# Optimization experiments

Measured on AMD Instinct MI355X. Metric: run time of the kernel, lower is better.

The kernel has to match this reference:

```python
import jax, jax.numpy as jnp
import numpy as np

H, W = 128, 128
TANFOVX = 0.5
TANFOVY = 0.5
SCALE_MOD = 1.0
NEAR = 0.2
N = 2048


def setup_inputs() -> dict:
    key = jax.random.key(0)
    ks = jax.random.split(key, 6)
    # Gaussians in front of an identity camera looking down +z
    xy = jax.random.uniform(ks[0], (N, 2), minval=-1.5, maxval=1.5)
    z = jax.random.uniform(ks[1], (N, 1), minval=2.5, maxval=6.5)
    means3D = jnp.concatenate([xy, z], axis=1).astype(jnp.float32)
    opacities = jax.random.uniform(ks[2], (N, 1), minval=0.05, maxval=0.95)
    colors_precomp = jax.random.uniform(ks[3], (N, 3))
    scales = jax.random.uniform(ks[4], (N, 3), minval=0.01, maxval=0.06)
    rotations = jax.random.normal(ks[5], (N, 4))
    viewmatrix = jnp.eye(4, dtype=jnp.float32)  # world == camera frame
    bg = jnp.zeros((3,), dtype=jnp.float32)
    return dict(means3D=means3D, opacities=opacities,
                colors_precomp=colors_precomp, scales=scales,
                rotations=rotations, viewmatrix=viewmatrix, bg=bg)


def _quat_to_rot(q):
    # normalized quaternion (w, x, y, z) -> rotation matrix, as in the CUDA kernel
    q = q / jnp.linalg.norm(q, axis=-1, keepdims=True)
    w, x, y, z = q[:, 0], q[:, 1], q[:, 2], q[:, 3]
    return jnp.stack([
        jnp.stack([1 - 2 * (y * y + z * z), 2 * (x * y - w * z), 2 * (x * z + w * y)], -1),
        jnp.stack([2 * (x * y + w * z), 1 - 2 * (x * x + z * z), 2 * (y * z - w * x)], -1),
        jnp.stack([2 * (x * z - w * y), 2 * (y * z + w * x), 1 - 2 * (x * x + y * y)], -1),
    ], -2)  # [N,3,3]


def _forward(means3D, opacities, colors_precomp, scales, rotations, viewmatrix, bg):
    fx = W / (2.0 * TANFOVX)
    fy = H / (2.0 * TANFOVY)
    Rv = viewmatrix[:3, :3]
    tv = viewmatrix[:3, 3]
    pv = means3D @ Rv.T + tv            # view-space positions [N,3]
    x, y, z = pv[:, 0], pv[:, 1], pv[:, 2]
    zc = jnp.maximum(z, 1e-4)
    # frustum clamping of the EWA Jacobian, as in forward.cu
    tx = jnp.clip(x / zc, -1.3 * TANFOVX, 1.3 * TANFOVX) * zc
    ty = jnp.clip(y / zc, -1.3 * TANFOVY, 1.3 * TANFOVY) * zc
    zeros = jnp.zeros_like(zc)
    J = jnp.stack([
        jnp.stack([fx / zc, zeros, -fx * tx / (zc * zc)], -1),
        jnp.stack([zeros, fy / zc, -fy * ty / (zc * zc)], -1),
    ], -2)                               # [N,2,3]
    # 3D covariance Sigma = R S S^T R^T
    Rg = _quat_to_rot(rotations)
    M = Rg * (scales * SCALE_MOD)[:, None, :]
    Sigma = M @ jnp.swapaxes(M, -1, -2)  # [N,3,3]
    T2 = jnp.einsum('nij,jk->nik', J, Rv)
    cov2d = jnp.einsum('nij,njk,nlk->nil', T2, Sigma, T2)
    a = cov2d[:, 0, 0] + 0.3             # low-pass filter, as in CUDA
    b = cov2d[:, 0, 1]
    c = cov2d[:, 1, 1] + 0.3
    det = a * c - b * b
    valid = (det > 0) & (z > NEAR)
    inv_det = jnp.where(det != 0, 1.0 / det, 0.0)
    conA, conB, conC = c * inv_det, -b * inv_det, a * inv_det
    mid = 0.5 * (a + c)
    lam = mid + jnp.sqrt(jnp.maximum(mid * mid - det, 0.1))
    radii = jnp.where(valid, jnp.ceil(3.0 * jnp.sqrt(lam)), 0.0)
    # projected pixel-space means
    mx = fx * (x / zc) + 0.5 * (W - 1)
    my = fy * (y / zc) + 0.5 * (H - 1)

    # global front-to-back depth sort (CUDA sorts per tile; one tile here)
    order = jnp.argsort(z)
    mx_s, my_s = mx[order], my[order]
    A_s, B_s, C_s = conA[order], conB[order], conC[order]
    op_s = opacities[order, 0]
    z_s = z[order]
    col_s = colors_precomp[order]
    valid_s = valid[order]

    px = jnp.arange(W, dtype=means3D.dtype)
    py = jnp.arange(H, dtype=means3D.dtype)
    Dx = mx_s[None, :] - px[:, None]     # [W,N]
    Dy = my_s[None, :] - py[:, None]     # [H,N]
    # power = -0.5 (A dx^2 + C dy^2) - B dx dy, built [H,W,N]
    power = (-0.5 * A_s * Dx * Dx)[None, :, :] \
            + (-0.5 * C_s * Dy * Dy)[:, None, :] \
            - (B_s * Dx)[None, :, :] * Dy[:, None, :]
    alpha = jnp.minimum(0.99, op_s * jnp.exp(jnp.minimum(power, 0.0)))
    alpha = jnp.where((power <= 0.0) & valid_s & (alpha >= 1.0 / 255.0), alpha, 0.0)
    alpha = alpha.reshape(H * W, N)      # [HW,N], front-to-back order
    logt = jnp.log1p(-alpha)
    csum = jnp.cumsum(logt, axis=-1)
    T_excl = jnp.exp(csum - logt)        # exclusive transmittance prod_{j<i}(1-a_j)
    wgt = alpha * T_excl                 # compositing weights
    T_final = jnp.exp(csum[:, -1])
    color = jnp.einsum('pn,nc->cp', wgt, col_s).reshape(3, H, W) \
            + T_final.reshape(1, H, W) * bg[:, None, None]
    depth = (wgt * z_s[None, :]).sum(-1).reshape(H, W)
    alpha_img = (1.0 - T_final).reshape(H, W)
    return color, radii, depth, alpha_img


def reference(means3D, opacities, colors_precomp, scales, rotations, viewmatrix, bg):
    return _forward(means3D, opacities, colors_precomp, scales, rotations, viewmatrix, bg)
```

## Files before the change

### kernel.cpp

```cpp
#include <hip/hip_runtime.h>

#define NG    2048
#define IMG_W 128
#define IMG_H 128
#define NPIX  (IMG_W * IMG_H)
#define REC   12

__global__ __launch_bounds__(64) void preprocess_kernel(
    const float* __restrict__ means,
    const float* __restrict__ opac,
    const float* __restrict__ cols,
    const float* __restrict__ scales,
    const float* __restrict__ rots,
    const float* __restrict__ vm4,
    float* __restrict__ u,
    float* __restrict__ zkey,
    float* __restrict__ radii_out)
{
    int i = blockIdx.x * 64 + threadIdx.x;
    if (i >= NG) return;

    const double fx = 128.0, fy = 128.0;

    double R00 = vm4[0], R01 = vm4[1], R02 = vm4[2],  t0 = vm4[3];
    double R10 = vm4[4], R11 = vm4[5], R12 = vm4[6],  t1 = vm4[7];
    double R20 = vm4[8], R21 = vm4[9], R22 = vm4[10], t2 = vm4[11];

    double m0 = means[3*i+0], m1 = means[3*i+1], m2 = means[3*i+2];
    double x = R00*m0 + R01*m1 + R02*m2 + t0;
    double y = R10*m0 + R11*m1 + R12*m2 + t1;
    double z = R20*m0 + R21*m1 + R22*m2 + t2;

    double zc   = fmax(z, 1e-4);
    double invz = 1.0 / zc;
    const double limx = 1.3 * 0.5, limy = 1.3 * 0.5;
    double tx = fmin(limx, fmax(-limx, x * invz)) * zc;
    double ty = fmin(limy, fmax(-limy, y * invz)) * zc;

    double J00 = fx * invz, J02 = -fx * tx * invz * invz;
    double J11 = fy * invz, J12 = -fy * ty * invz * invz;

    double qw = rots[4*i+0], qx = rots[4*i+1], qy = rots[4*i+2], qz = rots[4*i+3];
    double qn = 1.0 / sqrt(qw*qw + qx*qx + qy*qy + qz*qz);
    qw *= qn; qx *= qn; qy *= qn; qz *= qn;

    double Rg00 = 1.0 - 2.0*(qy*qy + qz*qz), Rg01 = 2.0*(qx*qy - qw*qz), Rg02 = 2.0*(qx*qz + qw*qy);
    double Rg10 = 2.0*(qx*qy + qw*qz), Rg11 = 1.0 - 2.0*(qx*qx + qz*qz), Rg12 = 2.0*(qy*qz - qw*qx);
    double Rg20 = 2.0*(qx*qz - qw*qy), Rg21 = 2.0*(qy*qz + qw*qx), Rg22 = 1.0 - 2.0*(qx*qx + qy*qy);

    double s0 = scales[3*i+0], s1 = scales[3*i+1], s2 = scales[3*i+2];
    double M00 = Rg00*s0, M01 = Rg01*s1, M02 = Rg02*s2;
    double M10 = Rg10*s0, M11 = Rg11*s1, M12 = Rg12*s2;
    double M20 = Rg20*s0, M21 = Rg21*s1, M22 = Rg22*s2;

    double S00 = M00*M00 + M01*M01 + M02*M02;
    double S01 = M00*M10 + M01*M11 + M02*M12;
    double S02 = M00*M20 + M01*M21 + M02*M22;
    double S11 = M10*M10 + M11*M11 + M12*M12;
    double S12 = M10*M20 + M11*M21 + M12*M22;
    double S22 = M20*M20 + M21*M21 + M22*M22;

    double Ta0 = J00*R00 + J02*R20, Ta1 = J00*R01 + J02*R21, Ta2 = J00*R02 + J02*R22;
    double Tb0 = J11*R10 + J12*R20, Tb1 = J11*R11 + J12*R21, Tb2 = J11*R12 + J12*R22;

    double Ua0 = Ta0*S00 + Ta1*S01 + Ta2*S02;
    double Ua1 = Ta0*S01 + Ta1*S11 + Ta2*S12;
    double Ua2 = Ta0*S02 + Ta1*S12 + Ta2*S22;
    double Ub0 = Tb0*S00 + Tb1*S01 + Tb2*S02;
    double Ub1 = Tb0*S01 + Tb1*S11 + Tb2*S12;
    double Ub2 = Tb0*S02 + Tb1*S12 + Tb2*S22;
    double cov00 = Ua0*Ta0 + Ua1*Ta1 + Ua2*Ta2;
    double cov01 = Ua0*Tb0 + Ua1*Tb1 + Ua2*Tb2;
    double cov11 = Ub0*Tb0 + Ub1*Tb1 + Ub2*Tb2;

    double a = cov00 + 0.3;
    double b = cov01;
    double c = cov11 + 0.3;
    double det = a*c - b*b;
    bool valid = (det > 0.0) && (z > 0.2);
    double inv_det = (det != 0.0) ? (1.0 / det) : 0.0;
    double conA =  c * inv_det;
    double conB = -b * inv_det;
    double conC =  a * inv_det;
    double mid = 0.5 * (a + c);
    double lam = mid + sqrt(fmax(mid*mid - det, 0.1));
    float radii = valid ? (float)ceil(3.0 * sqrt(lam)) : 0.0f;

    double mx = fx * (x * invz) + 0.5 * (IMG_W - 1);
    double my = fy * (y * invz) + 0.5 * (IMG_H - 1);

    double op = valid ? (double)opac[i] : 0.0;

    double r2c = -1.0;
    if (op > 0.0) {
        double lnterm = log(255.0 * op);
        if (lnterm > 0.0) r2c = 2.0 * lnterm * lam * 1.0001 + 1e-3;
    }

    u[i*REC + 0]  = (float)mx;
    u[i*REC + 1]  = (float)my;
    u[i*REC + 2]  = (float)conA;
    u[i*REC + 3]  = (float)conB;
    u[i*REC + 4]  = (float)conC;
    u[i*REC + 5]  = (float)op;
    u[i*REC + 6]  = (float)z;
    u[i*REC + 7]  = cols[3*i+0];
    u[i*REC + 8]  = cols[3*i+1];
    u[i*REC + 9]  = cols[3*i+2];
    u[i*REC + 10] = (float)r2c;
    u[i*REC + 11] = 0.0f;
    zkey[i]       = (float)z;
    radii_out[i]  = radii;
}

__global__ __launch_bounds__(256) void rank_scatter_kernel(
    const float* __restrict__ u,
    const float* __restrict__ zkey,
    float* __restrict__ s,
    float4* __restrict__ key4)
{
    __shared__ float zl[NG];
    int tid = threadIdx.x;
    for (int j = tid; j < NG; j += 256) zl[j] = zkey[j];
    __syncthreads();

    int g = tid >> 4;
    int p = tid & 15;
    int i = blockIdx.x * 16 + g;
    float zi = zl[i];

    const float4* z4 = (const float4*)zl;
    int rank = 0;
    #pragma unroll 4
    for (int it = 0; it < 32; ++it) {
        int idx = it * 16 + p;
        float4 f = z4[idx];
        int j0 = idx * 4;
        rank += (f.x < zi) || (f.x == zi && (j0 + 0) < i);
        rank += (f.y < zi) || (f.y == zi && (j0 + 1) < i);
        rank += (f.z < zi) || (f.z == zi && (j0 + 2) < i);
        rank += (f.w < zi) || (f.w == zi && (j0 + 3) < i);
    }
    rank += __shfl_down(rank, 8, 16);
    rank += __shfl_down(rank, 4, 16);
    rank += __shfl_down(rank, 2, 16);
    rank += __shfl_down(rank, 1, 16);

    if (p == 0) {
        const float4* src = (const float4*)(u + (size_t)i * REC);
        float4 a0 = src[0], a1 = src[1], a2 = src[2];
        float4* dst = (float4*)(s + (size_t)rank * REC);
        dst[0] = a0; dst[1] = a1; dst[2] = a2;
        key4[rank] = make_float4(a0.x, a0.y, a2.z, 0.0f);
    }
}

__global__ __launch_bounds__(256) void composite_kernel(
    const float* __restrict__ s,
    const float4* __restrict__ key4,
    const float* __restrict__ bg,
    float* __restrict__ out)
{
    __shared__ float comb[4 * 64 * 5];

    int tid  = threadIdx.x;
    int lane = tid & 63;
    int w    = tid >> 6;
    int tile = blockIdx.x;
    int x0 = (tile & 15) * 8;
    int y0 = (tile >> 4) * 8;
    float x0f = (float)x0,       y0f = (float)y0;
    float x1f = (float)(x0 + 7), y1f = (float)(y0 + 7);

    int px = x0 + (lane & 7);
    int py = y0 + (lane >> 3);
    float fpx = (float)px, fpy = (float)py;
    int p = py * IMG_W + px;

    float cr = 0.f, cg = 0.f, cb = 0.f, dep = 0.f, T = 1.f;

    const int SEG = NG / 4;
    int segbase = w * SEG;
    for (int c = 0; c < SEG; c += 64) {
        int gi = segbase + c + lane;
        float4 k4 = key4[gi];
        float ddx = fmaxf(0.f, fmaxf(x0f - k4.x, k4.x - x1f));
        float ddy = fmaxf(0.f, fmaxf(y0f - k4.y, k4.y - y1f));
        bool pass = (ddx*ddx + ddy*ddy) <= k4.z;

        unsigned long long m = __ballot(pass);
        float4 a0 = make_float4(0.f,0.f,0.f,0.f);
        float4 a1 = a0;
        float2 a2 = make_float2(0.f,0.f);
        if (pass) {
            const float* r = s + (size_t)gi * REC;
            a0 = *(const float4*)(r);
            a1 = *(const float4*)(r + 4);
            a2 = *(const float2*)(r + 8);
        }
        while (m) {
            int b = __ffsll(m) - 1;
            m &= m - 1;
            float mx = __shfl(a0.x, b);
            float my = __shfl(a0.y, b);
            float A  = __shfl(a0.z, b);
            float B  = __shfl(a0.w, b);
            float C  = __shfl(a1.x, b);
            float op = __shfl(a1.y, b);
            float gz = __shfl(a1.z, b);
            float gr = __shfl(a1.w, b);
            float gg = __shfl(a2.x, b);
            float gb = __shfl(a2.y, b);
            float dx = mx - fpx;
            float dy = my - fpy;
            float power = -0.5f * (A*dx*dx + C*dy*dy) - B*dx*dy;
            if (power <= 0.0f) {
                float al = fminf(0.99f, op * __expf(power));
                if (al >= (1.0f / 255.0f)) {
                    float wg = al * T;
                    dep += wg * gz;
                    cr  += wg * gr;
                    cg  += wg * gg;
                    cb  += wg * gb;
                    T *= (1.0f - al);
                }
            }
        }
    }

    int cb_base = (w * 64 + lane) * 5;
    comb[cb_base + 0] = cr;
    comb[cb_base + 1] = cg;
    comb[cb_base + 2] = cb;
    comb[cb_base + 3] = dep;
    comb[cb_base + 4] = T;
    __syncthreads();

    if (w == 0) {
        float CR = 0.f, CG = 0.f, CB = 0.f, DEP = 0.f, TT = 1.f;
        #pragma unroll
        for (int ww = 0; ww < 4; ++ww) {
            int b2 = (ww * 64 + lane) * 5;
            CR  += TT * comb[b2 + 0];
            CG  += TT * comb[b2 + 1];
            CB  += TT * comb[b2 + 2];
            DEP += TT * comb[b2 + 3];
            TT  *= comb[b2 + 4];
        }
        out[0*NPIX + p] = CR + TT * bg[0];
        out[1*NPIX + p] = CG + TT * bg[1];
        out[2*NPIX + p] = CB + TT * bg[2];
        out[3*NPIX + NG + p]        = DEP;
        out[3*NPIX + NG + NPIX + p] = 1.f - TT;
    }
}

extern "C" void kernel_launch(void* const* d_in, const int* in_sizes, int n_in,
                              void* d_out, int out_size, void* d_ws, size_t ws_size,
                              hipStream_t stream)
{
    const float* means = (const float*)d_in[0];
    const float* opac  = (const float*)d_in[1];
    const float* cols  = (const float*)d_in[2];
    const float* scl   = (const float*)d_in[3];
    const float* rot   = (const float*)d_in[4];
    const float* vm    = (const float*)d_in[5];
    const float* bg    = (const float*)d_in[6];
    float* out = (float*)d_out;

    float*  u    = (float*)d_ws;
    float*  zkey = u + NG * REC;
    float*  s    = zkey + NG;
    float4* key4 = (float4*)(s + NG * REC);

    preprocess_kernel<<<NG / 64, 64, 0, stream>>>(
        means, opac, cols, scl, rot, vm, u, zkey, out + 3 * NPIX);
    rank_scatter_kernel<<<NG / 16, 256, 0, stream>>>(u, zkey, s, key4);
    composite_kernel<<<NPIX / 64, 256, 0, stream>>>(s, key4, bg, out);
}
```

Measured before the change: 26.09 us.

## Fuse preprocess into rank kernel and batch culling ballots in composite

Merges the preprocess and rank/scatter kernels into one launch. Each block recomputes view-space depth for all Gaussians into shared memory, ranks them, then one lane per Gaussian runs the full preprocess and writes the sorted record directly, which removes the intermediate buffer and one kernel launch. The composite kernel now computes all eight tile-culling ballots up front, and it loads the color and depth shuffles only when some lane in the wave actually contributes. The cost is redundant depth recomputation in every block and a serial preprocess done by only one lane out of sixteen.

```diff
diff --git a/kernel.cpp b/kernel.cpp
--- a/kernel.cpp
+++ b/kernel.cpp
@@ -6,25 +6,55 @@
 #define NPIX  (IMG_W * IMG_H)
 #define REC   12
 
-__global__ __launch_bounds__(64) void preprocess_kernel(
+__global__ __launch_bounds__(256) void prep_rank_kernel(
     const float* __restrict__ means,
     const float* __restrict__ opac,
     const float* __restrict__ cols,
     const float* __restrict__ scales,
     const float* __restrict__ rots,
     const float* __restrict__ vm4,
-    float* __restrict__ u,
-    float* __restrict__ zkey,
+    float* __restrict__ s,
+    float4* __restrict__ key4,
     float* __restrict__ radii_out)
 {
-    int i = blockIdx.x * 64 + threadIdx.x;
-    if (i >= NG) return;
+    __shared__ __align__(16) float zl[NG];
+    int tid = threadIdx.x;
 
     const double fx = 128.0, fy = 128.0;
 
     double R00 = vm4[0], R01 = vm4[1], R02 = vm4[2],  t0 = vm4[3];
     double R10 = vm4[4], R11 = vm4[5], R12 = vm4[6],  t1 = vm4[7];
     double R20 = vm4[8], R21 = vm4[9], R22 = vm4[10], t2 = vm4[11];
+
+    for (int j = tid; j < NG; j += 256) {
+        double zj = R20*means[3*j] + R21*means[3*j+1] + R22*means[3*j+2] + t2;
+        zl[j] = (float)zj;
+    }
+    __syncthreads();
+
+    int g = tid >> 4;
+    int p = tid & 15;
+    int i = blockIdx.x * 16 + g;
+    float zi = zl[i];
+
+    const float4* z4 = (const float4*)zl;
+    int rank = 0;
+    #pragma unroll 4
+    for (int it = 0; it < 32; ++it) {
+        int idx = it * 16 + p;
+        float4 f = z4[idx];
+        int j0 = idx * 4;
+        rank += (f.x < zi) || (f.x == zi && (j0 + 0) < i);
+        rank += (f.y < zi) || (f.y == zi && (j0 + 1) < i);
+        rank += (f.z < zi) || (f.z == zi && (j0 + 2) < i);
+        rank += (f.w < zi) || (f.w == zi && (j0 + 3) < i);
+    }
+    rank += __shfl_down(rank, 8, 16);
+    rank += __shfl_down(rank, 4, 16);
+    rank += __shfl_down(rank, 2, 16);
+    rank += __shfl_down(rank, 1, 16);
+
+    if (p != 0) return;
 
     double m0 = means[3*i+0], m1 = means[3*i+1], m2 = means[3*i+2];
     double x = R00*m0 + R01*m1 + R02*m2 + t0;
@@ -97,62 +127,12 @@
         if (lnterm > 0.0) r2c = 2.0 * lnterm * lam * 1.0001 + 1e-3;
     }
 
-    u[i*REC + 0]  = (float)mx;
-    u[i*REC + 1]  = (float)my;
-    u[i*REC + 2]  = (float)conA;
-    u[i*REC + 3]  = (float)conB;
-    u[i*REC + 4]  = (float)conC;
-    u[i*REC + 5]  = (float)op;
-    u[i*REC + 6]  = (float)z;
-    u[i*REC + 7]  = cols[3*i+0];
-    u[i*REC + 8]  = cols[3*i+1];
-    u[i*REC + 9]  = cols[3*i+2];
-    u[i*REC + 10] = (float)r2c;
-    u[i*REC + 11] = 0.0f;
-    zkey[i]       = (float)z;
-    radii_out[i]  = radii;
-}
-
-__global__ __launch_bounds__(256) void rank_scatter_kernel(
-    const float* __restrict__ u,
-    const float* __restrict__ zkey,
-    float* __restrict__ s,
-    float4* __restrict__ key4)
-{
-    __shared__ float zl[NG];
-    int tid = threadIdx.x;
-    for (int j = tid; j < NG; j += 256) zl[j] = zkey[j];
-    __syncthreads();
-
-    int g = tid >> 4;
-    int p = tid & 15;
-    int i = blockIdx.x * 16 + g;
-    float zi = zl[i];
-
-    const float4* z4 = (const float4*)zl;
-    int rank = 0;
-    #pragma unroll 4
-    for (int it = 0; it < 32; ++it) {
-        int idx = it * 16 + p;
-        float4 f = z4[idx];
-        int j0 = idx * 4;
-        rank += (f.x < zi) || (f.x == zi && (j0 + 0) < i);
-        rank += (f.y < zi) || (f.y == zi && (j0 + 1) < i);
-        rank += (f.z < zi) || (f.z == zi && (j0 + 2) < i);
-        rank += (f.w < zi) || (f.w == zi && (j0 + 3) < i);
-    }
-    rank += __shfl_down(rank, 8, 16);
-    rank += __shfl_down(rank, 4, 16);
-    rank += __shfl_down(rank, 2, 16);
-    rank += __shfl_down(rank, 1, 16);
-
-    if (p == 0) {
-        const float4* src = (const float4*)(u + (size_t)i * REC);
-        float4 a0 = src[0], a1 = src[1], a2 = src[2];
-        float4* dst = (float4*)(s + (size_t)rank * REC);
-        dst[0] = a0; dst[1] = a1; dst[2] = a2;
-        key4[rank] = make_float4(a0.x, a0.y, a2.z, 0.0f);
-    }
+    float* dst = s + (size_t)rank * REC;
+    *(float4*)(dst)     = make_float4((float)mx, (float)my, (float)conA, (float)conB);
+    *(float4*)(dst + 4) = make_float4((float)conC, (float)op, (float)z, cols[3*i+0]);
+    *(float4*)(dst + 8) = make_float4(cols[3*i+1], cols[3*i+2], (float)r2c, 0.0f);
+    key4[rank]   = make_float4((float)mx, (float)my, (float)r2c, 0.0f);
+    radii_out[i] = radii;
 }
 
 __global__ __launch_bounds__(256) void composite_kernel(
@@ -177,53 +157,61 @@
     float fpx = (float)px, fpy = (float)py;
     int p = py * IMG_W + px;
 
-    float cr = 0.f, cg = 0.f, cb = 0.f, dep = 0.f, T = 1.f;
-
     const int SEG = NG / 4;
     int segbase = w * SEG;
-    for (int c = 0; c < SEG; c += 64) {
-        int gi = segbase + c + lane;
-        float4 k4 = key4[gi];
+
+    unsigned long long m[8];
+    unsigned pb = 0;
+    #pragma unroll
+    for (int c = 0; c < 8; ++c) {
+        float4 k4 = key4[segbase + c * 64 + lane];
         float ddx = fmaxf(0.f, fmaxf(x0f - k4.x, k4.x - x1f));
         float ddy = fmaxf(0.f, fmaxf(y0f - k4.y, k4.y - y1f));
         bool pass = (ddx*ddx + ddy*ddy) <= k4.z;
-
-        unsigned long long m = __ballot(pass);
+        m[c] = __ballot(pass);
+        pb |= pass ? (1u << c) : 0u;
+    }
+
+    float cr = 0.f, cg = 0.f, cb = 0.f, dep = 0.f, T = 1.f;
+
+    #pragma unroll
+    for (int c = 0; c < 8; ++c) {
+        unsigned long long mm = m[c];
+        if (!mm) continue;
         float4 a0 = make_float4(0.f,0.f,0.f,0.f);
         float4 a1 = a0;
         float2 a2 = make_float2(0.f,0.f);
-        if (pass) {
-            const float* r = s + (size_t)gi * REC;
+        if ((pb >> c) & 1u) {
+            const float* r = s + (size_t)(segbase + c * 64 + lane) * REC;
             a0 = *(const float4*)(r);
             a1 = *(const float4*)(r + 4);
             a2 = *(const float2*)(r + 8);
         }
-        while (m) {
-            int b = __ffsll(m) - 1;
-            m &= m - 1;
+        while (mm) {
+            int b = __ffsll(mm) - 1;
+            mm &= mm - 1;
             float mx = __shfl(a0.x, b);
             float my = __shfl(a0.y, b);
             float A  = __shfl(a0.z, b);
             float B  = __shfl(a0.w, b);
             float C  = __shfl(a1.x, b);
             float op = __shfl(a1.y, b);
-            float gz = __shfl(a1.z, b);
-            float gr = __shfl(a1.w, b);
-            float gg = __shfl(a2.x, b);
-            float gb = __shfl(a2.y, b);
             float dx = mx - fpx;
             float dy = my - fpy;
             float power = -0.5f * (A*dx*dx + C*dy*dy) - B*dx*dy;
-            if (power <= 0.0f) {
-                float al = fminf(0.99f, op * __expf(power));
-                if (al >= (1.0f / 255.0f)) {
-                    float wg = al * T;
-                    dep += wg * gz;
-                    cr  += wg * gr;
-                    cg  += wg * gg;
-                    cb  += wg * gb;
-                    T *= (1.0f - al);
-                }
+            float al = fminf(0.99f, op * __expf(power));
+            bool take = (power <= 0.0f) && (al >= (1.0f / 255.0f));
+            if (__any(take)) {
+                float gz = __shfl(a1.z, b);
+                float gr = __shfl(a1.w, b);
+                float gg = __shfl(a2.x, b);
+                float gb = __shfl(a2.y, b);
+                float wgt = take ? al * T : 0.0f;
+                dep += wgt * gz;
+                cr  += wgt * gr;
+                cg  += wgt * gg;
+                cb  += wgt * gb;
+                if (take) T *= (1.0f - al);
             }
         }
     }
@@ -268,13 +256,10 @@
     const float* bg    = (const float*)d_in[6];
     float* out = (float*)d_out;
 
-    float*  u    = (float*)d_ws;
-    float*  zkey = u + NG * REC;
-    float*  s    = zkey + NG;
+    float*  s    = (float*)d_ws;
     float4* key4 = (float4*)(s + NG * REC);
 
-    preprocess_kernel<<<NG / 64, 64, 0, stream>>>(
-        means, opac, cols, scl, rot, vm, u, zkey, out + 3 * NPIX);
-    rank_scatter_kernel<<<NG / 16, 256, 0, stream>>>(u, zkey, s, key4);
+    prep_rank_kernel<<<NG / 16, 256, 0, stream>>>(
+        means, opac, cols, scl, rot, vm, s, key4, out + 3 * NPIX);
     composite_kernel<<<NPIX / 64, 256, 0, stream>>>(s, key4, bg, out);
 }
```

Result: faster. 23.22 us (-11.0%).
